# Performance work log

Hardware: AMD Instinct MI355X
Metric: run time of the kernel (lower is better)

Reference implementation:

```python
import jax, jax.numpy as jnp
import numpy as np

D_HEAD = 64
IGNORE = -100000.0


def setup_inputs() -> dict:
    key = jax.random.key(0)
    ks = jax.random.split(key, 5)
    B, S, D, H, M = 2, 2048, 768, 12, D_HEAD
    scale = 0.05  # 'random_normal' keras init stddev
    return {
        "x": jax.random.normal(ks[0], (B, S, D), jnp.float32),
        "W_Q": jax.random.normal(ks[1], (H, D, M), jnp.float32) * scale,
        "b_Q": jnp.zeros((H, M), jnp.float32),
        "W_K": jax.random.normal(ks[2], (H, D, M), jnp.float32) * scale,
        "b_K": jnp.zeros((H, M), jnp.float32),
        "W_V": jax.random.normal(ks[3], (H, D, M), jnp.float32) * scale,
        "b_V": jnp.zeros((H, M), jnp.float32),
        "W_O": jax.random.normal(ks[4], (H, M, D), jnp.float32) * scale,
        "b_O": jnp.zeros((D,), jnp.float32),
    }


def reference(x, W_Q, b_Q, W_K, b_K, W_V, b_V, W_O, b_O):
    # q,k,v: [b, s, h, m]
    q = jnp.einsum("bqd,hdm->bqhm", x, W_Q) + b_Q
    k = jnp.einsum("bkd,hdm->bkhm", x, W_K) + b_K
    v = jnp.einsum("bkd,hdm->bkhm", x, W_V) + b_V
    # scores: [b, h, q, k], scaled by 1/sqrt(d_head)
    scores = jnp.einsum("bqhm,bkhm->bhqk", q, k) / jnp.sqrt(
        jnp.asarray(D_HEAD, q.dtype)
    )
    S = x.shape[1]
    # causal mask: strictly-upper-triangular positions set to IGNORE (-1e5),
    # matching tf.where(mask == 1, IGNORE, scores)
    causal = jnp.arange(S)[:, None] >= jnp.arange(S)[None, :]  # [q, k]
    scores = jnp.where(causal[None, None, :, :], scores, jnp.asarray(IGNORE, scores.dtype))
    pattern = jax.nn.softmax(scores, axis=-1)
    z = jnp.einsum("bhqk,bkhm->bqhm", pattern, v)
    attn_out = jnp.einsum("bqhm,hmd->bqd", z, W_O) + b_O
    return attn_out
```

## Files before the change

### kernel.cpp

```cpp
#include <hip/hip_runtime.h>
#include <hip/hip_bf16.h>
#include <cstdint>
#include <cstddef>

#define B_ 2
#define S_ 2048
#define D_ 768
#define H_ 12
#define M_ 64
#define BS_ (B_ * S_)
#define NQKV_ 2304
#define NCHUNK_ 80
#define TOTCHUNK_ (24 * NCHUNK_)
#define QSCALE 0.18033688011f

typedef __attribute__((ext_vector_type(8))) short bf16x8;
typedef __attribute__((ext_vector_type(4))) short bf16x4;
typedef __attribute__((ext_vector_type(4))) float f32x4;

__device__ __forceinline__ unsigned short f2bu(float f) {
    __hip_bfloat16 h = __float2bfloat16(f);
    unsigned short u;
    __builtin_memcpy(&u, &h, 2);
    return u;
}
__device__ __forceinline__ unsigned pack2(float a, float b) {
    return (unsigned)f2bu(a) | ((unsigned)f2bu(b) << 16);
}

__device__ __forceinline__ bf16x8 ld16(const unsigned short* p) {
    p = (const unsigned short*)__builtin_assume_aligned(p, 16);
    bf16x8 v; __builtin_memcpy(&v, p, 16); return v;
}
__device__ __forceinline__ bf16x4 ld8(const unsigned short* p) {
    p = (const unsigned short*)__builtin_assume_aligned(p, 8);
    bf16x4 v; __builtin_memcpy(&v, p, 8); return v;
}
__device__ __forceinline__ uint4 ld16u(const unsigned short* p) {
    p = (const unsigned short*)__builtin_assume_aligned(p, 16);
    uint4 v; __builtin_memcpy(&v, p, 16); return v;
}
__device__ __forceinline__ void st16(unsigned short* p, uint4 v) {
    p = (unsigned short*)__builtin_assume_aligned(p, 16);
    __builtin_memcpy(p, &v, 16);
}
__device__ __forceinline__ void st8(unsigned short* p, uint2 v) {
    p = (unsigned short*)__builtin_assume_aligned(p, 8);
    __builtin_memcpy(p, &v, 8);
}
__device__ __forceinline__ float4 ldf4(const float* p) {
    p = (const float*)__builtin_assume_aligned(p, 16);
    float4 v; __builtin_memcpy(&v, p, 16); return v;
}
__device__ __forceinline__ void async16(const unsigned short* g, unsigned short* l) {
    __builtin_amdgcn_global_load_lds(
        (const __attribute__((address_space(1))) void*)g,
        (__attribute__((address_space(3))) void*)l, 16, 0, 0);
}
__device__ __forceinline__ void b82f(uint4 u, float* o) {
    o[0] = __uint_as_float(u.x << 16); o[1] = __uint_as_float(u.x & 0xffff0000u);
    o[2] = __uint_as_float(u.y << 16); o[3] = __uint_as_float(u.y & 0xffff0000u);
    o[4] = __uint_as_float(u.z << 16); o[5] = __uint_as_float(u.z & 0xffff0000u);
    o[6] = __uint_as_float(u.w << 16); o[7] = __uint_as_float(u.w & 0xffff0000u);
}

#define NEG_BIG (-3.0e38f)

__global__ void prep(const float* __restrict__ WQ, const float* __restrict__ WK,
                     const float* __restrict__ WV, const float* __restrict__ WO,
                     const float* __restrict__ x,
                     unsigned short* __restrict__ WT,
                     unsigned short* __restrict__ WOT,
                     unsigned short* __restrict__ xb)
{
    const int bx = blockIdx.x;
    if (bx < 216) {
        const int xx = bx % 9, yy = bx / 9;
        const int c  = xx * 256 + threadIdx.x;
        const int k0 = yy * 32;
        const int which = c / D_;
        const int r = c - which * D_;
        const int h = r >> 6, m = r & 63;
        const float* Wsel = (which == 0) ? WQ : (which == 1) ? WK : WV;
        const float* src = Wsel + (size_t)h * D_ * M_ + m;
        unsigned short* dst = WT + (size_t)c * D_ + k0;
        for (int i = 0; i < 32; i += 8) {
            float wv[8];
#pragma unroll
            for (int j = 0; j < 8; j++) wv[j] = src[(size_t)(k0 + i + j) * M_];
            uint4 pu;
            pu.x = pack2(wv[0], wv[1]); pu.y = pack2(wv[2], wv[3]);
            pu.z = pack2(wv[4], wv[5]); pu.w = pack2(wv[6], wv[7]);
            st16(dst + i, pu);
        }
    } else if (bx < 288) {
        const int b2 = bx - 216;
        const int xx = b2 % 3, yy = b2 / 3;
        const int c  = xx * 256 + threadIdx.x;
        const int k0 = yy * 32;
        unsigned short* dst = WOT + (size_t)c * D_ + k0;
        for (int i = 0; i < 32; i += 8) {
            float wv[8];
#pragma unroll
            for (int j = 0; j < 8; j++) wv[j] = WO[(size_t)(k0 + i + j) * D_ + c];
            uint4 pu;
            pu.x = pack2(wv[0], wv[1]); pu.y = pack2(wv[2], wv[3]);
            pu.z = pack2(wv[4], wv[5]); pu.w = pack2(wv[6], wv[7]);
            st16(dst + i, pu);
        }
    } else {
        const size_t i = ((size_t)(bx - 288) * 256 + threadIdx.x) * 16;
#pragma unroll
        for (int p = 0; p < 2; p++) {
            float4 a0 = ldf4(x + i + p * 8), a1 = ldf4(x + i + p * 8 + 4);
            uint4 u;
            u.x = pack2(a0.x, a0.y); u.y = pack2(a0.z, a0.w);
            u.z = pack2(a1.x, a1.y); u.w = pack2(a1.z, a1.w);
            st16(xb + i + p * 8, u);
        }
    }
}

__global__ __launch_bounds__(256, 2) void qkv_gemm(
    const unsigned short* __restrict__ xb,
    const unsigned short* __restrict__ WT,
    const float* __restrict__ bQ, const float* __restrict__ bK,
    const float* __restrict__ bV,
    unsigned short* __restrict__ qo, unsigned short* __restrict__ ko,
    unsigned short* __restrict__ vt)
{
    const int row0 = blockIdx.x * 128;
    const int col0 = blockIdx.y * 128;
    const int t = threadIdx.x;
    const int w = t >> 6, lane = t & 63, quad = lane >> 4, l16 = lane & 15;
    const int wrow0 = (w & 1) * 64, wcol0 = (w >> 1) * 64;

    __shared__ unsigned short Alds[128 * 64];
    __shared__ unsigned short Blds[128 * 64];

    f32x4 acc[4][4] = {};

    const unsigned short* asrc[4];
    const unsigned short* bsrc[4];
    int ldsoff[4];
#pragma unroll
    for (int q = 0; q < 4; q++) {
        const int cq = w * 256 + q * 64 + lane;
        const int row = cq >> 3, c = cq & 7;
        const int cs = c ^ (row & 7);
        asrc[q] = xb + (size_t)(row0 + row) * D_ + cs * 8;
        bsrc[q] = WT + (size_t)(col0 + row) * D_ + cs * 8;
        ldsoff[q] = (w * 256 + q * 64) * 8;
    }
    const int swz = (l16 & 7);

    for (int k0 = 0; k0 < D_; k0 += 64) {
#pragma unroll
        for (int q = 0; q < 4; q++) async16(asrc[q] + k0, Alds + ldsoff[q]);
#pragma unroll
        for (int q = 0; q < 4; q++) async16(bsrc[q] + k0, Blds + ldsoff[q]);
        __syncthreads();

        bf16x8 af[4][2], bfm[4][2];
#pragma unroll
        for (int rt = 0; rt < 4; rt++) {
            const int row = wrow0 + rt * 16 + l16;
#pragma unroll
            for (int hh = 0; hh < 2; hh++)
                af[rt][hh] = ld16(&Alds[row * 64 + ((hh * 4 + quad) ^ swz) * 8]);
        }
#pragma unroll
        for (int st = 0; st < 4; st++) {
            const int row = wcol0 + st * 16 + l16;
#pragma unroll
            for (int hh = 0; hh < 2; hh++)
                bfm[st][hh] = ld16(&Blds[row * 64 + ((hh * 4 + quad) ^ swz) * 8]);
        }
#pragma unroll
        for (int rt = 0; rt < 4; rt++)
#pragma unroll
            for (int st = 0; st < 4; st++) {
                acc[rt][st] = __builtin_amdgcn_mfma_f32_16x16x32_bf16(
                    af[rt][0], bfm[st][0], acc[rt][st], 0, 0, 0);
                acc[rt][st] = __builtin_amdgcn_mfma_f32_16x16x32_bf16(
                    af[rt][1], bfm[st][1], acc[rt][st], 0, 0, 0);
            }
        __syncthreads();
    }

    const int which = col0 / D_;
    const int colin = col0 - which * D_;

    if (which < 2) {
        const float* bias = (which == 0) ? bQ : bK;
        unsigned short* outp = (which == 0) ? qo : ko;
        const float scale = (which == 0) ? QSCALE : 1.0f;
#pragma unroll
        for (int st = 0; st < 4; st++) {
            const int cl = colin + wcol0 + st * 16 + l16;
            const int h = cl >> 6, m = cl & 63;
            const float bval = bias[cl];
#pragma unroll
            for (int rt = 0; rt < 4; rt++)
#pragma unroll
                for (int rr = 0; rr < 4; rr++) {
                    const int R = row0 + wrow0 + rt * 16 + quad * 4 + rr;
                    const int bb = R >> 11, s = R & (S_ - 1);
                    outp[(((size_t)bb * H_ + h) * S_ + s) * M_ + m] =
                        f2bu((acc[rt][st][rr] + bval) * scale);
                }
        }
    } else {
#pragma unroll
        for (int st = 0; st < 4; st++) {
            const int cl = colin + wcol0 + st * 16 + l16;
            const int h = cl >> 6, m = cl & 63;
            const float bval = bV[cl];
#pragma unroll
            for (int rt = 0; rt < 4; rt++) {
                const int R0 = row0 + wrow0 + rt * 16 + quad * 4;
                const int bb = R0 >> 11, s0 = R0 & (S_ - 1);
                uint2 v;
                v.x = pack2(acc[rt][st][0] + bval, acc[rt][st][1] + bval);
                v.y = pack2(acc[rt][st][2] + bval, acc[rt][st][3] + bval);
                st8(&vt[(((size_t)bb * H_ + h) * M_ + m) * S_ + s0], v);
            }
        }
    }
}

struct StageRegs { uint4 ka[4]; uint4 va[4]; };

__device__ __forceinline__ void load_tile(const unsigned short* kb,
                                          const unsigned short* vb,
                                          int t, StageRegs& s)
{
#pragma unroll
    for (int q = 0; q < 4; q++) {
        const int ci = q * 256 + t;
        s.ka[q] = ld16u(kb + (size_t)(ci >> 3) * M_ + (ci & 7) * 8);
    }
#pragma unroll
    for (int q = 0; q < 4; q++) {
        const int ci = q * 256 + t;
        s.va[q] = ld16u(vb + (size_t)(ci >> 4) * S_ + (ci & 15) * 8);
    }
}

__global__ __launch_bounds__(256, 2) void attn_split(
    const unsigned short* __restrict__ Q,
    const unsigned short* __restrict__ Kin,
    const unsigned short* __restrict__ Vt,
    unsigned short* __restrict__ Opart,
    float* __restrict__ ml)
{
    const int flat = blockIdx.y * NCHUNK_ + blockIdx.x;
    const int bh = flat % 24;
    const int xx = (NCHUNK_ - 1) - flat / 24;

    int qt, c, nc;
    if (xx < 8)       { qt = xx; c = 0; nc = 1; }
    else if (xx < 24) { int u = xx - 8;  qt = 8  + (u >> 1); c = u & 1;  nc = 2; }
    else if (xx < 48) { int u = xx - 24; qt = 16 + u / 3;    c = u % 3;  nc = 3; }
    else              { int u = xx - 48; qt = 24 + (u >> 2); c = u & 3;  nc = 4; }

    const int ci     = bh * NCHUNK_ + xx;
    const int kbeg   = c * 512;
    const int keyend = min((qt + 1) * 64, kbeg + 512);
    const int iters  = (keyend - kbeg + 127) >> 7;
    const bool lastchunk = (c == nc - 1);

    const int t = threadIdx.x;
    const int wave = t >> 6, lane = t & 63, quad = lane >> 4, l16 = lane & 15;

    const unsigned short* Qb  = Q   + ((size_t)bh * S_ + qt * 64) * M_;
    const unsigned short* Kb  = Kin + (size_t)bh * S_ * M_;
    const unsigned short* VtB = Vt  + (size_t)bh * M_ * S_;

    __shared__ unsigned short Klds[128 * 64];
    __shared__ unsigned short Vlds[64 * 128];

    bf16x8 qf[2];
    {
        const unsigned short* qrow = Qb + (size_t)(wave * 16 + l16) * M_;
        qf[0] = ld16(qrow + quad * 8);
        qf[1] = ld16(qrow + 32 + quad * 8);
    }

    const int ksw = l16 & 7;
    const int ko0 = (quad ^ ksw) * 8;
    const int ko1 = ((quad + 4) ^ ksw) * 8;
    int voff[8];
#pragma unroll
    for (int st = 0; st < 8; st++)
        voff[st] = l16 * 128 + (quad ^ (l16 & 3)) * 4
                 + ((st ^ ((l16 >> 2) & 3)) << 4);

    f32x4 o_acc[4] = {};
    float lrow = 0.f;

    StageRegs sr;
    load_tile(Kb + (size_t)kbeg * M_, VtB + kbeg, t, sr);

    for (int it = 0; it < iters; it++) {
        __syncthreads();
#pragma unroll
        for (int q = 0; q < 4; q++) {
            const int cq = q * 256 + t;
            const int row = cq >> 3;
            const int bp = (cq & 7) ^ (row & 7);
            st16(&Klds[row * 64 + bp * 8], sr.ka[q]);
        }
#pragma unroll
        for (int q = 0; q < 4; q++) {
            const int cq = q * 256 + t;
            const int f = cq >> 4, pl = cq & 15;
            const int pp = pl ^ ((f >> 1) & 7);
            uint4 v = sr.va[q];
            if (f & 1) {
                unsigned tx = v.x, ty = v.y;
                v.x = v.z; v.y = v.w; v.z = tx; v.w = ty;
            }
            st16(&Vlds[f * 128 + pp * 8], v);
        }
        __syncthreads();

        if (it + 1 < iters) {
            const int key1 = kbeg + (it + 1) * 128;
            load_tile(Kb + (size_t)key1 * M_, VtB + key1, t, sr);
        }

        f32x4 s_acc[8];
#pragma unroll
        for (int st = 0; st < 8; st++) {
            f32x4 z4 = {0.f, 0.f, 0.f, 0.f};
            const unsigned short* krow = &Klds[(st * 16 + l16) * 64];
            bf16x8 k0 = ld16(krow + ko0);
            bf16x8 k1 = ld16(krow + ko1);
            z4 = __builtin_amdgcn_mfma_f32_16x16x32_bf16(k0, qf[0], z4, 0, 0, 0);
            z4 = __builtin_amdgcn_mfma_f32_16x16x32_bf16(k1, qf[1], z4, 0, 0, 0);
            s_acc[st] = z4;
        }

        if (lastchunk && it == iters - 1) {
            const int keyq = kbeg + it * 128 + quad * 4;
            const int qg = qt * 64 + wave * 16 + l16;
#pragma unroll
            for (int st = 0; st < 8; st++)
#pragma unroll
                for (int r = 0; r < 4; r++)
                    if (keyq + st * 16 + r > qg)
                        s_acc[st][r] = -1e30f;
        }

        bf16x4 pkv[8];
#pragma unroll
        for (int st = 0; st < 8; st++) {
            float p0 = exp2f(s_acc[st][0]);
            float p1 = exp2f(s_acc[st][1]);
            float p2 = exp2f(s_acc[st][2]);
            float p3 = exp2f(s_acc[st][3]);
            lrow += (p0 + p1) + (p2 + p3);
            uint2 u;
            u.x = pack2(p0, p1);
            u.y = pack2(p2, p3);
            __builtin_memcpy(&pkv[st], &u, 8);
        }

#pragma unroll
        for (int stf = 0; stf < 4; stf++) {
#pragma unroll
            for (int st = 0; st < 8; st++) {
                bf16x4 va = ld8(&Vlds[stf * 2048 + voff[st]]);
                o_acc[stf] = __builtin_amdgcn_mfma_f32_16x16x16bf16_1k(
                    va, pkv[st], o_acc[stf], 0, 0, 0);
            }
        }
    }

    lrow += __shfl_xor(lrow, 16, 64);
    lrow += __shfl_xor(lrow, 32, 64);

    unsigned short* Op = Opart + (size_t)ci * 4096;
    const int q = wave * 16 + l16;
#pragma unroll
    for (int stf = 0; stf < 4; stf++) {
        uint2 u;
        u.x = pack2(o_acc[stf][0], o_acc[stf][1]);
        u.y = pack2(o_acc[stf][2], o_acc[stf][3]);
        st8(&Op[q * 64 + stf * 16 + quad * 4], u);
    }
    if (quad == 0)
        ml[(size_t)ci * 128 + 64 + q] = lrow;
}

__global__ void combine(const unsigned short* __restrict__ Opart,
                        const float* __restrict__ ml,
                        unsigned short* __restrict__ Z)
{
    const int qt = blockIdx.x, bh = blockIdx.y;
    const int b = bh / H_, h = bh - b * H_;
    const int g = qt >> 3, r7 = qt & 7;
    const int nc = g + 1;
    const int base = bh * NCHUNK_ + qt + 4 * g * (g - 1) + r7 * g;

    const int t = threadIdx.x;
    const int q = t >> 2, fs = (t & 3) * 16;

    float L = 0.f;
    for (int c = 0; c < nc; c++)
        L += ml[(size_t)(base + c) * 128 + 64 + q];
    const float invL = 1.0f / L;

    float o[16] = {};
    for (int c = 0; c < nc; c++) {
        const unsigned short* op =
            Opart + (size_t)(base + c) * 4096 + q * 64 + fs;
        float f[8];
        b82f(ld16u(op), f);
#pragma unroll
        for (int j = 0; j < 8; j++) o[j] += f[j];
        b82f(ld16u(op + 8), f);
#pragma unroll
        for (int j = 0; j < 8; j++) o[8 + j] += f[j];
    }

    unsigned short* zp =
        Z + ((size_t)b * S_ + qt * 64 + q) * (H_ * M_) + h * M_ + fs;
    uint4 u0, u1;
    u0.x = pack2(o[0]*invL,  o[1]*invL);  u0.y = pack2(o[2]*invL,  o[3]*invL);
    u0.z = pack2(o[4]*invL,  o[5]*invL);  u0.w = pack2(o[6]*invL,  o[7]*invL);
    u1.x = pack2(o[8]*invL,  o[9]*invL);  u1.y = pack2(o[10]*invL, o[11]*invL);
    u1.z = pack2(o[12]*invL, o[13]*invL); u1.w = pack2(o[14]*invL, o[15]*invL);
    st16(zp, u0);
    st16(zp + 8, u1);
}

__global__ __launch_bounds__(256, 2) void oproj_gemm(
    const unsigned short* __restrict__ Zin,
    const unsigned short* __restrict__ WOT,
    const float* __restrict__ bO,
    float* __restrict__ out)
{
    const int row0 = blockIdx.x * 128;
    const int col0 = blockIdx.y * 128;
    const int t = threadIdx.x;
    const int w = t >> 6, lane = t & 63, quad = lane >> 4, l16 = lane & 15;
    const int wrow0 = (w & 1) * 64, wcol0 = (w >> 1) * 64;

    __shared__ unsigned short Alds[128 * 64];
    __shared__ unsigned short Blds[128 * 64];

    f32x4 acc[4][4] = {};

    const unsigned short* asrc[4];
    const unsigned short* bsrc[4];
    int ldsoff[4];
#pragma unroll
    for (int q = 0; q < 4; q++) {
        const int cq = w * 256 + q * 64 + lane;
        const int row = cq >> 3, c = cq & 7;
        const int cs = c ^ (row & 7);
        asrc[q] = Zin + (size_t)(row0 + row) * D_ + cs * 8;
        bsrc[q] = WOT + (size_t)(col0 + row) * D_ + cs * 8;
        ldsoff[q] = (w * 256 + q * 64) * 8;
    }
    const int swz = (l16 & 7);

    for (int k0 = 0; k0 < D_; k0 += 64) {
#pragma unroll
        for (int q = 0; q < 4; q++) async16(asrc[q] + k0, Alds + ldsoff[q]);
#pragma unroll
        for (int q = 0; q < 4; q++) async16(bsrc[q] + k0, Blds + ldsoff[q]);
        __syncthreads();

        bf16x8 af[4][2], bfm[4][2];
#pragma unroll
        for (int rt = 0; rt < 4; rt++) {
            const int row = wrow0 + rt * 16 + l16;
#pragma unroll
            for (int hh = 0; hh < 2; hh++)
                af[rt][hh] = ld16(&Alds[row * 64 + ((hh * 4 + quad) ^ swz) * 8]);
        }
#pragma unroll
        for (int st = 0; st < 4; st++) {
            const int row = wcol0 + st * 16 + l16;
#pragma unroll
            for (int hh = 0; hh < 2; hh++)
                bfm[st][hh] = ld16(&Blds[row * 64 + ((hh * 4 + quad) ^ swz) * 8]);
        }
#pragma unroll
        for (int rt = 0; rt < 4; rt++)
#pragma unroll
            for (int st = 0; st < 4; st++) {
                acc[rt][st] = __builtin_amdgcn_mfma_f32_16x16x32_bf16(
                    af[rt][0], bfm[st][0], acc[rt][st], 0, 0, 0);
                acc[rt][st] = __builtin_amdgcn_mfma_f32_16x16x32_bf16(
                    af[rt][1], bfm[st][1], acc[rt][st], 0, 0, 0);
            }
        __syncthreads();
    }

#pragma unroll
    for (int st = 0; st < 4; st++) {
        const int c = col0 + wcol0 + st * 16 + l16;
        const float bval = bO[c];
#pragma unroll
        for (int rt = 0; rt < 4; rt++)
#pragma unroll
            for (int rr = 0; rr < 4; rr++) {
                const int R = row0 + wrow0 + rt * 16 + quad * 4 + rr;
                out[(size_t)R * D_ + c] = acc[rt][st][rr] + bval;
            }
    }
}

extern "C" void kernel_launch(void* const* d_in, const int* in_sizes, int n_in,
                              void* d_out, int out_size, void* d_ws, size_t ws_size,
                              hipStream_t stream)
{
    const float* x  = (const float*)d_in[0];
    const float* WQ = (const float*)d_in[1];
    const float* bQ = (const float*)d_in[2];
    const float* WK = (const float*)d_in[3];
    const float* bK = (const float*)d_in[4];
    const float* WV = (const float*)d_in[5];
    const float* bV = (const float*)d_in[6];
    const float* WO = (const float*)d_in[7];
    const float* bO = (const float*)d_in[8];
    float* out = (float*)d_out;

    const size_t n = (size_t)B_ * H_ * S_ * M_;
    unsigned short* q_ws  = (unsigned short*)d_ws;
    unsigned short* k_ws  = q_ws + n;
    unsigned short* vt_ws = k_ws + n;
    unsigned short* z_ws  = vt_ws + n;
    unsigned short* WT    = z_ws + n;
    unsigned short* WOT   = WT + (size_t)NQKV_ * D_;
    unsigned short* xb    = WOT + (size_t)D_ * D_;
    unsigned short* Opart = xb + (size_t)BS_ * D_;
    float* mlbuf = (float*)(Opart + (size_t)TOTCHUNK_ * 4096);

    prep<<<dim3(1056), 256, 0, stream>>>(WQ, WK, WV, WO, x, WT, WOT, xb);
    qkv_gemm<<<dim3(BS_ / 128, NQKV_ / 128), 256, 0, stream>>>(
        xb, WT, bQ, bK, bV, q_ws, k_ws, vt_ws);
    attn_split<<<dim3(NCHUNK_, B_ * H_), 256, 0, stream>>>(
        q_ws, k_ws, vt_ws, Opart, mlbuf);
    combine<<<dim3(S_ / 64, B_ * H_), 256, 0, stream>>>(Opart, mlbuf, z_ws);
    oproj_gemm<<<dim3(BS_ / 128, D_ / 128), 256, 0, stream>>>(
        z_ws, WOT, bO, out);
}
```

Baseline: 160.8 us.

## Pre-swizzle K and V layouts in projection and load tiles via async LDS copies

The QKV projection now writes K with an XOR-swizzled column order and V in per-128-key tiles already arranged in the LDS layout the attention kernel expects. The attention kernel can then copy contiguous tiles straight into LDS with async global-to-LDS loads, dropping the register staging, shuffling and LDS stores. This removes instruction and VGPR overhead but also drops the software prefetch of the next tile, so load latency is no longer overlapped with compute across iterations.

```diff
diff --git a/kernel.cpp b/kernel.cpp
--- a/kernel.cpp
+++ b/kernel.cpp
@@ -191,23 +191,38 @@
     const int which = col0 / D_;
     const int colin = col0 - which * D_;
 
-    if (which < 2) {
-        const float* bias = (which == 0) ? bQ : bK;
-        unsigned short* outp = (which == 0) ? qo : ko;
-        const float scale = (which == 0) ? QSCALE : 1.0f;
+    if (which == 0) {
 #pragma unroll
         for (int st = 0; st < 4; st++) {
             const int cl = colin + wcol0 + st * 16 + l16;
             const int h = cl >> 6, m = cl & 63;
-            const float bval = bias[cl];
+            const float bval = bQ[cl];
 #pragma unroll
             for (int rt = 0; rt < 4; rt++)
 #pragma unroll
                 for (int rr = 0; rr < 4; rr++) {
                     const int R = row0 + wrow0 + rt * 16 + quad * 4 + rr;
                     const int bb = R >> 11, s = R & (S_ - 1);
-                    outp[(((size_t)bb * H_ + h) * S_ + s) * M_ + m] =
-                        f2bu((acc[rt][st][rr] + bval) * scale);
+                    qo[(((size_t)bb * H_ + h) * S_ + s) * M_ + m] =
+                        f2bu((acc[rt][st][rr] + bval) * QSCALE);
+                }
+        }
+    } else if (which == 1) {
+#pragma unroll
+        for (int st = 0; st < 4; st++) {
+            const int cl = colin + wcol0 + st * 16 + l16;
+            const int h = cl >> 6, m = cl & 63;
+            const int blk = m >> 3, inn = m & 7;
+            const float bval = bK[cl];
+#pragma unroll
+            for (int rt = 0; rt < 4; rt++)
+#pragma unroll
+                for (int rr = 0; rr < 4; rr++) {
+                    const int R = row0 + wrow0 + rt * 16 + quad * 4 + rr;
+                    const int bb = R >> 11, s = R & (S_ - 1);
+                    ko[(((size_t)bb * H_ + h) * S_ + s) * M_ +
+                       ((blk ^ (s & 7)) << 3) + inn] =
+                        f2bu(acc[rt][st][rr] + bval);
                 }
         }
     } else {
@@ -220,30 +235,18 @@
             for (int rt = 0; rt < 4; rt++) {
                 const int R0 = row0 + wrow0 + rt * 16 + quad * 4;
                 const int bb = R0 >> 11, s0 = R0 & (S_ - 1);
+                const int tile = s0 >> 7;
+                const int gl = (s0 & 127) >> 2;
+                const int pl = gl >> 1, hi = gl & 1;
+                const int pp = pl ^ ((m >> 1) & 7);
+                const int half = hi ^ (m & 1);
                 uint2 v;
                 v.x = pack2(acc[rt][st][0] + bval, acc[rt][st][1] + bval);
                 v.y = pack2(acc[rt][st][2] + bval, acc[rt][st][3] + bval);
-                st8(&vt[(((size_t)bb * H_ + h) * M_ + m) * S_ + s0], v);
+                st8(&vt[(((size_t)bb * H_ + h) * 16 + tile) * (M_ * 128)
+                        + m * 128 + (pp * 2 + half) * 4], v);
             }
         }
-    }
-}
-
-struct StageRegs { uint4 ka[4]; uint4 va[4]; };
-
-__device__ __forceinline__ void load_tile(const unsigned short* kb,
-                                          const unsigned short* vb,
-                                          int t, StageRegs& s)
-{
-#pragma unroll
-    for (int q = 0; q < 4; q++) {
-        const int ci = q * 256 + t;
-        s.ka[q] = ld16u(kb + (size_t)(ci >> 3) * M_ + (ci & 7) * 8);
-    }
-#pragma unroll
-    for (int q = 0; q < 4; q++) {
-        const int ci = q * 256 + t;
-        s.va[q] = ld16u(vb + (size_t)(ci >> 4) * S_ + (ci & 15) * 8);
     }
 }
 
@@ -275,7 +278,7 @@
 
     const unsigned short* Qb  = Q   + ((size_t)bh * S_ + qt * 64) * M_;
     const unsigned short* Kb  = Kin + (size_t)bh * S_ * M_;
-    const unsigned short* VtB = Vt  + (size_t)bh * M_ * S_;
+    const unsigned short* Vb  = Vt  + (size_t)bh * M_ * S_;
 
     __shared__ unsigned short Klds[128 * 64];
     __shared__ unsigned short Vlds[64 * 128];
@@ -296,39 +299,23 @@
         voff[st] = l16 * 128 + (quad ^ (l16 & 3)) * 4
                  + ((st ^ ((l16 >> 2) & 3)) << 4);
 
+    const int wdst = wave * 64 * 8;
+
     f32x4 o_acc[4] = {};
     float lrow = 0.f;
 
-    StageRegs sr;
-    load_tile(Kb + (size_t)kbeg * M_, VtB + kbeg, t, sr);
-
     for (int it = 0; it < iters; it++) {
         __syncthreads();
-#pragma unroll
-        for (int q = 0; q < 4; q++) {
-            const int cq = q * 256 + t;
-            const int row = cq >> 3;
-            const int bp = (cq & 7) ^ (row & 7);
-            st16(&Klds[row * 64 + bp * 8], sr.ka[q]);
-        }
-#pragma unroll
-        for (int q = 0; q < 4; q++) {
-            const int cq = q * 256 + t;
-            const int f = cq >> 4, pl = cq & 15;
-            const int pp = pl ^ ((f >> 1) & 7);
-            uint4 v = sr.va[q];
-            if (f & 1) {
-                unsigned tx = v.x, ty = v.y;
-                v.x = v.z; v.y = v.w; v.z = tx; v.w = ty;
-            }
-            st16(&Vlds[f * 128 + pp * 8], v);
-        }
+        const int key0 = kbeg + it * 128;
+        const unsigned short* kt = Kb + (size_t)key0 * M_;
+        const unsigned short* vtile = Vb + (size_t)(key0 >> 7) * (M_ * 128);
+#pragma unroll
+        for (int q = 0; q < 4; q++)
+            async16(kt + (size_t)(q * 256 + t) * 8, Klds + q * 2048 + wdst);
+#pragma unroll
+        for (int q = 0; q < 4; q++)
+            async16(vtile + (size_t)(q * 256 + t) * 8, Vlds + q * 2048 + wdst);
         __syncthreads();
-
-        if (it + 1 < iters) {
-            const int key1 = kbeg + (it + 1) * 128;
-            load_tile(Kb + (size_t)key1 * M_, VtB + key1, t, sr);
-        }
 
         f32x4 s_acc[8];
 #pragma unroll
```

New measurement: 158.3 us. About the same (-1.5%).
